# Kernel tuning notes

Measured on AMD Instinct MI355X. Metric: run time of the kernel, lower is better.

Reference implementation:

```python
import jax, jax.numpy as jnp
import numpy as np

B, S, E, H, FFN, NQ = 4, 2048, 1024, 16, 4096, 8
DK = E // H
EPS = 1e-5


def setup_inputs() -> dict:
    key = jax.random.key(0)
    ks = jax.random.split(key, 8)
    x = jax.random.normal(ks[0], (B, S, E), dtype=jnp.float32)
    theta = jax.random.normal(ks[1], (NQ,), dtype=jnp.float32)  # RY angles
    w1 = jax.random.normal(ks[2], (FFN, NQ), dtype=jnp.float32) / np.sqrt(NQ)
    b1 = jnp.zeros((FFN,), dtype=jnp.float32)
    w2 = jax.random.normal(ks[3], (E, FFN), dtype=jnp.float32) / np.sqrt(FFN)
    b2 = jnp.zeros((E,), dtype=jnp.float32)
    gamma1 = jnp.ones((E,), dtype=jnp.float32)
    beta1 = jnp.zeros((E,), dtype=jnp.float32)
    gamma2 = jnp.ones((E,), dtype=jnp.float32)
    beta2 = jnp.zeros((E,), dtype=jnp.float32)
    return {"x": x, "theta": theta, "w1": w1, "b1": b1, "w2": w2, "b2": b2,
            "gamma1": gamma1, "beta1": beta1, "gamma2": gamma2, "beta2": beta2}


def _layernorm(h, g, b):
    mu = jnp.mean(h, axis=-1, keepdims=True)
    var = jnp.mean(jnp.square(h - mu), axis=-1, keepdims=True)
    return (h - mu) * jax.lax.rsqrt(var + EPS) * g + b


def _attention(x):
    # q = k = v = separate_heads(x); no projection weights in the original.
    q = x.reshape(B, S, H, DK).transpose(0, 2, 1, 3)  # [B,H,S,DK]
    scores = jnp.einsum("bhqd,bhkd->bhqk", q, q) / np.sqrt(DK)
    probs = jax.nn.softmax(scores, axis=-1)
    out = jnp.einsum("bhqk,bhkd->bhqd", probs, q)
    return out.transpose(0, 2, 1, 3).reshape(B, S, E)


def _ffn_quantum(h, theta, w1, b1, w2, b2):
    # Per-token circuit: RX(x_i) then RY(theta_i) on independent qubits,
    # measure PauliZ -> <Z_i> = cos(x_i) * cos(theta_i). Batched over all tokens.
    qout = jnp.cos(h[..., :NQ]) * jnp.cos(theta)  # [B,S,NQ]
    hid = jax.nn.relu(jnp.einsum("bsq,fq->bsf", qout, w1) + b1)
    return jnp.einsum("bsf,ef->bse", hid, w2) + b2


def reference(x, theta, w1, b1, w2, b2, gamma1, beta1, gamma2, beta2):
    attn_out = _attention(x)
    h = _layernorm(x + attn_out, gamma1, beta1)
    ffn_out = _ffn_quantum(h, theta, w1, b1, w2, b2)
    return _layernorm(h + ffn_out, gamma2, beta2)
```

## Files before the change

### kernel.cpp

```cpp
#include <hip/hip_runtime.h>


#define Bq 4
#define Sq 2048
#define Eq 1024
#define Hq 16
#define DKq 64
#define FFNq 4096
#define NQq 8
#define LOG2E 1.44269504f

typedef unsigned int u32;
typedef unsigned short u16;
typedef _Float16 f16;
typedef f16 f16x8 __attribute__((ext_vector_type(8)));
typedef __fp16 fp16x2 __attribute__((ext_vector_type(2)));
typedef float f32x4 __attribute__((ext_vector_type(4)));

#if __has_builtin(__builtin_amdgcn_exp2f)
#define EXP2F __builtin_amdgcn_exp2f
#else
#define EXP2F exp2f
#endif

#define MFMA(a, b, c) __builtin_amdgcn_mfma_f32_16x16x32_f16((a), (b), (c), 0, 0, 0)

#define GLL(g, l)                                                          \
  __builtin_amdgcn_global_load_lds(                                        \
      (const __attribute__((address_space(1))) u32*)(g),                   \
      (__attribute__((address_space(3))) u32*)(l), 16, 0, 0)

__device__ __forceinline__ u16 f2h(float x) {
  f16 t = (f16)x;
  return __builtin_bit_cast(u16, t);
}
__device__ __forceinline__ float h2f(u16 w) {
  return (float)__builtin_bit_cast(f16, w);
}
#if __has_builtin(__builtin_amdgcn_cvt_pkrtz)
__device__ __forceinline__ u32 pkrtz(float a, float b) {
  fp16x2 r = __builtin_amdgcn_cvt_pkrtz(a, b);
  return __builtin_bit_cast(u32, r);
}
#else
__device__ __forceinline__ u32 pkrtz(float a, float b) {
  return (u32)f2h(a) | ((u32)f2h(b) << 16);
}
#endif

union F8 { f16x8 v; u32 w[4]; u16 h[8]; f16 e[8]; };

__global__ void k_cvt(const float* __restrict__ src, uint4* __restrict__ dst, int n8) {
  int i = blockIdx.x * 256 + threadIdx.x;
  if (i >= n8) return;
  const float4* s = (const float4*)src + 2 * (long)i;
  float4 a = s[0], b = s[1];
  uint4 r;
  r.x = pkrtz(a.x, a.y);
  r.y = pkrtz(a.z, a.w);
  r.z = pkrtz(b.x, b.y);
  r.w = pkrtz(b.z, b.w);
  dst[i] = r;
}

__global__ void k_prep(const float* __restrict__ x, u16* __restrict__ xh,
                       u16* __restrict__ xt) {
  __shared__ u16 tile[64 * 72];
  const int tid = threadIdx.x;
  const int bx = blockIdx.x;
  const int sb = bx & 31, bh = bx >> 5;
  const int b = bh >> 4, h = bh & 15;
  const int s0 = sb * 64;
  const int r = tid >> 2, cq = tid & 3;
  const float* xp = x + ((long)(b * Sq + s0 + r)) * Eq + h * 64 + cq * 16;
  float4 f0 = ((const float4*)xp)[0], f1 = ((const float4*)xp)[1];
  float4 f2 = ((const float4*)xp)[2], f3 = ((const float4*)xp)[3];
  u32 w[8];
  w[0] = pkrtz(f0.x, f0.y); w[1] = pkrtz(f0.z, f0.w);
  w[2] = pkrtz(f1.x, f1.y); w[3] = pkrtz(f1.z, f1.w);
  w[4] = pkrtz(f2.x, f2.y); w[5] = pkrtz(f2.z, f2.w);
  w[6] = pkrtz(f3.x, f3.y); w[7] = pkrtz(f3.z, f3.w);
  uint4* xo = (uint4*)(xh + ((long)(b * Sq + s0 + r)) * Eq + h * 64 + cq * 16);
  xo[0] = make_uint4(w[0], w[1], w[2], w[3]);
  xo[1] = make_uint4(w[4], w[5], w[6], w[7]);
  uint4* tp = (uint4*)(tile + r * 72 + cq * 16);
  tp[0] = make_uint4(w[0], w[1], w[2], w[3]);
  tp[1] = make_uint4(w[4], w[5], w[6], w[7]);
  __syncthreads();
  const int d = tid >> 2, rq = tid & 3;
  u32 o[8];
#pragma unroll
  for (int i = 0; i < 8; ++i) {
    u32 lo = tile[(rq * 16 + 2 * i) * 72 + d];
    u32 hi = tile[(rq * 16 + 2 * i + 1) * 72 + d];
    o[i] = lo | (hi << 16);
  }
  uint4* to = (uint4*)(xt + ((long)(bh * 64 + d)) * Sq + s0 + rq * 16);
  to[0] = make_uint4(o[0], o[1], o[2], o[3]);
  to[1] = make_uint4(o[4], o[5], o[6], o[7]);
}

__global__ __launch_bounds__(256) void k_attn(const u16* __restrict__ xh,
                                              const u16* __restrict__ xt,
                                              u16* __restrict__ attn) {
  __shared__ __align__(16) u16 lds[16384];
  u16* Kl = lds;
  u16* Vt = lds + 4096;
  u16* Pl = lds + 8192;

  const int tid = threadIdx.x;
  const int wave = tid >> 6, lane = tid & 63;
  const int n = lane & 15, quad = lane >> 4;

  const int bx = blockIdx.x;
  const int qb = bx >> 6, bh = bx & 63;
  const int b = bh >> 4, h = bh & 15;

  const u16* xh_bh = xh + (long)b * Sq * Eq + h * 64;
  const u16* xt_bh = xt + (long)bh * 64 * Sq;

  const float SC = 0.125f * LOG2E;
  F8 qf[2][2];
  float shift[2];
#pragma unroll
  for (int nt = 0; nt < 2; ++nt) {
    const int q = qb * 128 + wave * 32 + nt * 16 + n;
    const u16* qp = xh_bh + (long)q * Eq + quad * 8;
    F8 a, c;
    a.v = *(const f16x8*)qp;
    c.v = *(const f16x8*)(qp + 32);
    float s2 = 0.f;
#pragma unroll
    for (int i = 0; i < 8; ++i) {
      float va = (float)a.e[i], vc = (float)c.e[i];
      s2 += va * va + vc * vc;
      qf[nt][0].e[i] = a.e[i] * (f16)SC;
      qf[nt][1].e[i] = c.e[i] * (f16)SC;
    }
    s2 += __shfl_xor(s2, 16);
    s2 += __shfl_xor(s2, 32);
    shift[nt] = SC * s2;
  }

  const int r8 = lane >> 3;
  const int cl = (lane & 7) ^ r8;
  const u16* gK0 = xh_bh + (long)(wave * 16 + r8) * Eq + cl * 8;
  const u16* gK1 = gK0 + 8 * Eq;
  const u16* gV0 = xt_bh + (long)(wave * 16 + r8) * Sq + cl * 8;
  const u16* gV1 = gV0 + 8 * Sq;
  u16* lK0 = Kl + wave * 1024;
  u16* lK1 = lK0 + 512;
  u16* lV0 = Vt + wave * 1024;
  u16* lV1 = lV0 + 512;

  f32x4 O[2][4] = {};
  f32x4 lC[2] = {};
  const f16x8 vones = {(f16)1, (f16)1, (f16)1, (f16)1,
                       (f16)1, (f16)1, (f16)1, (f16)1};
  u16* Pw0 = Pl + (wave * 2 + 0) * 1024;
  u16* Pw1 = Pl + (wave * 2 + 1) * 1024;

  for (int kb = 0; kb < Sq / 64; ++kb) {
    __syncthreads();
    GLL(gK0, lK0); GLL(gK1, lK1);
    GLL(gV0, lV0); GLL(gV1, lV1);
    gK0 += 64 * Eq; gK1 += 64 * Eq; gV0 += 64; gV1 += 64;
    __syncthreads();

    f32x4 ST[2][4];
#pragma unroll
    for (int nt = 0; nt < 2; ++nt) {
      const float ms = -shift[nt];
#pragma unroll
      for (int mt = 0; mt < 4; ++mt) {
        ST[nt][mt][0] = ms; ST[nt][mt][1] = ms;
        ST[nt][mt][2] = ms; ST[nt][mt][3] = ms;
      }
    }
#pragma unroll
    for (int mt = 0; mt < 4; ++mt) {
#pragma unroll
      for (int c = 0; c < 2; ++c) {
        f16x8 af = *(const f16x8*)(Kl + (mt * 16 + n) * 64 +
                                   (((c * 4 + quad) ^ (n & 7)) * 8));
        ST[0][mt] = MFMA(af, qf[0][c].v, ST[0][mt]);
        ST[1][mt] = MFMA(af, qf[1][c].v, ST[1][mt]);
      }
    }

#pragma unroll
    for (int nt = 0; nt < 2; ++nt) {
      u16* Pw = nt ? Pw1 : Pw0;
#pragma unroll
      for (int mt = 0; mt < 4; ++mt) {
        float p0 = EXP2F(ST[nt][mt][0]);
        float p1 = EXP2F(ST[nt][mt][1]);
        float p2 = EXP2F(ST[nt][mt][2]);
        float p3 = EXP2F(ST[nt][mt][3]);
        const int ch = 2 * mt + (quad >> 1);
        *(uint2*)(Pw + n * 64 + ((ch ^ (n & 7)) * 8) + (quad & 1) * 4) =
            make_uint2(pkrtz(p0, p1), pkrtz(p2, p3));
      }
    }

#pragma unroll
    for (int c = 0; c < 2; ++c) {
      const int pc = ((c * 4 + quad) ^ (n & 7)) * 8;
      f16x8 pf0 = *(const f16x8*)(Pw0 + n * 64 + pc);
      f16x8 pf1 = *(const f16x8*)(Pw1 + n * 64 + pc);
      lC[0] = MFMA(vones, pf0, lC[0]);
      lC[1] = MFMA(vones, pf1, lC[1]);
#pragma unroll
      for (int dt = 0; dt < 4; ++dt) {
        f16x8 vf = *(const f16x8*)(Vt + (dt * 16 + n) * 64 + pc);
        O[0][dt] = MFMA(vf, pf0, O[0][dt]);
        O[1][dt] = MFMA(vf, pf1, O[1][dt]);
      }
    }
  }

#pragma unroll
  for (int nt = 0; nt < 2; ++nt) {
    const float inv = 1.0f / lC[nt][0];
    const int q = qb * 128 + wave * 32 + nt * 16 + n;
    u16* op = attn + (long)b * Sq * Eq + (long)q * Eq + h * 64;
#pragma unroll
    for (int dt = 0; dt < 4; ++dt) {
      u32 w0 = pkrtz(O[nt][dt][0] * inv, O[nt][dt][1] * inv);
      u32 w1 = pkrtz(O[nt][dt][2] * inv, O[nt][dt][3] * inv);
      *(uint2*)(op + dt * 16 + quad * 4) = make_uint2(w0, w1);
    }
  }
}

__global__ void k_ln1(const u16* __restrict__ xh, const u16* __restrict__ attn,
                      const float* __restrict__ g, const float* __restrict__ be,
                      const float* __restrict__ theta, u16* __restrict__ hout,
                      u16* __restrict__ qout) {
  const long t = blockIdx.x;
  const int tid = threadIdx.x;
  uint2 xw = ((const uint2*)(xh + t * Eq))[tid];
  uint2 aw = ((const uint2*)(attn + t * Eq))[tid];
  float v0 = h2f(xw.x & 0xffff) + h2f(aw.x & 0xffff);
  float v1 = h2f(xw.x >> 16) + h2f(aw.x >> 16);
  float v2 = h2f(xw.y & 0xffff) + h2f(aw.y & 0xffff);
  float v3 = h2f(xw.y >> 16) + h2f(aw.y >> 16);
  float s = (v0 + v1) + (v2 + v3);
  float s2 = v0 * v0 + v1 * v1 + v2 * v2 + v3 * v3;
#pragma unroll
  for (int o = 1; o < 64; o <<= 1) {
    s += __shfl_xor(s, o);
    s2 += __shfl_xor(s2, o);
  }
  __shared__ float red[8];
  const int wv = tid >> 6, ln = tid & 63;
  if (ln == 0) { red[wv] = s; red[4 + wv] = s2; }
  __syncthreads();
  s = red[0] + red[1] + red[2] + red[3];
  s2 = red[4] + red[5] + red[6] + red[7];
  const float mu = s * (1.f / Eq);
  const float var = s2 * (1.f / Eq) - mu * mu;
  const float rstd = rsqrtf(var + 1e-5f);
  float4 gv = ((const float4*)g)[tid];
  float4 bv = ((const float4*)be)[tid];
  float o0 = (v0 - mu) * rstd * gv.x + bv.x;
  float o1 = (v1 - mu) * rstd * gv.y + bv.y;
  float o2 = (v2 - mu) * rstd * gv.z + bv.z;
  float o3 = (v3 - mu) * rstd * gv.w + bv.w;
  ((uint2*)(hout + t * Eq))[tid] = make_uint2(pkrtz(o0, o1), pkrtz(o2, o3));
  if (tid < 2) {
    float hv[4] = {o0, o1, o2, o3};
    float q[4];
#pragma unroll
    for (int i = 0; i < 4; ++i) q[i] = cosf(hv[i]) * cosf(theta[tid * 4 + i]);
    *(uint2*)(qout + t * NQq + tid * 4) = make_uint2(pkrtz(q[0], q[1]), pkrtz(q[2], q[3]));
  }
}

__global__ void k_hid(const u16* __restrict__ qout, const float* __restrict__ w1,
                      const float* __restrict__ b1, u16* __restrict__ hid) {
  __shared__ float qs[256][8];
  const int tid = threadIdx.x;
  const int fb = blockIdx.x & 63, tb = blockIdx.x >> 6;
  const int f0 = fb * 64, t0 = tb * 256;
  {
    uint4 qw = *(const uint4*)(qout + (long)(t0 + tid) * NQq);
    qs[tid][0] = h2f(qw.x & 0xffff); qs[tid][1] = h2f(qw.x >> 16);
    qs[tid][2] = h2f(qw.y & 0xffff); qs[tid][3] = h2f(qw.y >> 16);
    qs[tid][4] = h2f(qw.z & 0xffff); qs[tid][5] = h2f(qw.z >> 16);
    qs[tid][6] = h2f(qw.w & 0xffff); qs[tid][7] = h2f(qw.w >> 16);
  }
  __syncthreads();
  const int wave = tid >> 6, lane = tid & 63;
  const int f = f0 + lane;
  const float4* wp = (const float4*)(w1 + (long)f * NQq);
  float4 wa = wp[0], wb = wp[1];
  const float bb = b1[f];
  const int trow = wave * 64;
  u16* op = hid + (long)(t0 + trow) * FFNq + f;
#pragma unroll 4
  for (int i = 0; i < 64; ++i) {
    const float* q = qs[trow + i];
    float acc = bb + q[0] * wa.x + q[1] * wa.y + q[2] * wa.z + q[3] * wa.w +
                q[4] * wb.x + q[5] * wb.y + q[6] * wb.z + q[7] * wb.w;
    acc = fmaxf(acc, 0.f);
    op[(long)i * FFNq] = f2h(acc);
  }
}

__global__ __launch_bounds__(256) void k_gemm(const u16* __restrict__ Ah,
                                              const u16* __restrict__ Bh,
                                              u16* __restrict__ C0,
                                              u16* __restrict__ C1) {
  __shared__ __align__(16) u16 lds[16384];
  u16* La = lds;
  u16* Lb = lds + 8192;
  const int tid = threadIdx.x;
  const int wave = tid >> 6, lane = tid & 63;
  const int n = lane & 15, quad = lane >> 4;
  const int wm = wave >> 1, wn = wave & 1;
  const int bxx = blockIdx.x;
  const int kk = bxx >> 9;
  const int bx = bxx & 511;
  const int m0 = (bx >> 3) * 128;
  const int n0 = (bx & 7) * 128;
  const int k0 = kk * (FFNq / 2);
  const int r8 = lane >> 3;
  const int cl = (lane & 7) ^ r8;

  const u16* gA[4];
  const u16* gB[4];
  u16* lA[4];
  u16* lB[4];
#pragma unroll
  for (int j = 0; j < 4; ++j) {
    const int row = wave * 32 + j * 8;
    gA[j] = Ah + (long)(m0 + row + r8) * FFNq + k0 + cl * 8;
    gB[j] = Bh + (long)(n0 + row + r8) * FFNq + k0 + cl * 8;
    lA[j] = La + row * 64;
    lB[j] = Lb + row * 64;
  }

  f32x4 acc[4][4] = {};
  for (int it = 0; it < FFNq / 2 / 64; ++it) {
    __syncthreads();
#pragma unroll
    for (int j = 0; j < 4; ++j) {
      GLL(gA[j], lA[j]);
      GLL(gB[j], lB[j]);
      gA[j] += 64;
      gB[j] += 64;
    }
    __syncthreads();
#pragma unroll
    for (int c = 0; c < 2; ++c) {
      f16x8 af[4], bf[4];
#pragma unroll
      for (int i = 0; i < 4; ++i) {
        const int ra = wm * 64 + i * 16 + n;
        const int rb = wn * 64 + i * 16 + n;
        af[i] = *(const f16x8*)(La + ra * 64 + (((c * 4 + quad) ^ (n & 7)) * 8));
        bf[i] = *(const f16x8*)(Lb + rb * 64 + (((c * 4 + quad) ^ (n & 7)) * 8));
      }
#pragma unroll
      for (int i = 0; i < 4; ++i)
#pragma unroll
        for (int j = 0; j < 4; ++j) acc[i][j] = MFMA(af[i], bf[j], acc[i][j]);
    }
  }
  u16* C = kk ? C1 : C0;
#pragma unroll
  for (int i = 0; i < 4; ++i) {
    const int row = m0 + wm * 64 + i * 16 + quad * 4;
#pragma unroll
    for (int j = 0; j < 4; ++j) {
      u16* cp = C + (long)row * Eq + n0 + wn * 64 + j * 16 + n;
      cp[0] = f2h(acc[i][j][0]);
      cp[Eq] = f2h(acc[i][j][1]);
      cp[2 * Eq] = f2h(acc[i][j][2]);
      cp[3 * Eq] = f2h(acc[i][j][3]);
    }
  }
}

__global__ void k_ln2(const u16* __restrict__ hin, const u16* __restrict__ p0f,
                      const u16* __restrict__ p1f, const float* __restrict__ b2,
                      const float* __restrict__ g, const float* __restrict__ be,
                      float* __restrict__ out) {
  const long t = blockIdx.x;
  const int tid = threadIdx.x;
  uint2 hw = ((const uint2*)(hin + t * Eq))[tid];
  uint2 fw = ((const uint2*)(p0f + t * Eq))[tid];
  uint2 ew = ((const uint2*)(p1f + t * Eq))[tid];
  float4 b2v = ((const float4*)b2)[tid];
  float v0 = h2f(hw.x & 0xffff) + h2f(fw.x & 0xffff) + h2f(ew.x & 0xffff) + b2v.x;
  float v1 = h2f(hw.x >> 16) + h2f(fw.x >> 16) + h2f(ew.x >> 16) + b2v.y;
  float v2 = h2f(hw.y & 0xffff) + h2f(fw.y & 0xffff) + h2f(ew.y & 0xffff) + b2v.z;
  float v3 = h2f(hw.y >> 16) + h2f(fw.y >> 16) + h2f(ew.y >> 16) + b2v.w;
  float s = (v0 + v1) + (v2 + v3);
  float s2 = v0 * v0 + v1 * v1 + v2 * v2 + v3 * v3;
#pragma unroll
  for (int o = 1; o < 64; o <<= 1) {
    s += __shfl_xor(s, o);
    s2 += __shfl_xor(s2, o);
  }
  __shared__ float red[8];
  const int wv = tid >> 6, ln = tid & 63;
  if (ln == 0) { red[wv] = s; red[4 + wv] = s2; }
  __syncthreads();
  s = red[0] + red[1] + red[2] + red[3];
  s2 = red[4] + red[5] + red[6] + red[7];
  const float mu = s * (1.f / Eq);
  const float var = s2 * (1.f / Eq) - mu * mu;
  const float rstd = rsqrtf(var + 1e-5f);
  float4 gv = ((const float4*)g)[tid];
  float4 bv = ((const float4*)be)[tid];
  float4 o;
  o.x = (v0 - mu) * rstd * gv.x + bv.x;
  o.y = (v1 - mu) * rstd * gv.y + bv.y;
  o.z = (v2 - mu) * rstd * gv.z + bv.z;
  o.w = (v3 - mu) * rstd * gv.w + bv.w;
  ((float4*)(out + t * Eq))[tid] = o;
}

extern "C" void kernel_launch(void* const* d_in, const int* in_sizes, int n_in,
                              void* d_out, int out_size, void* d_ws, size_t ws_size,
                              hipStream_t stream) {
  const float* x = (const float*)d_in[0];
  const float* theta = (const float*)d_in[1];
  const float* w1 = (const float*)d_in[2];
  const float* b1 = (const float*)d_in[3];
  const float* w2 = (const float*)d_in[4];
  const float* b2 = (const float*)d_in[5];
  const float* g1 = (const float*)d_in[6];
  const float* be1 = (const float*)d_in[7];
  const float* g2 = (const float*)d_in[8];
  const float* be2 = (const float*)d_in[9];
  float* out = (float*)d_out;

  char* ws = (char*)d_ws;
  u16* attn = (u16*)(ws);
  u16* h = (u16*)(ws + 16777216);
  u16* xh = (u16*)(ws + 33554432);
  u16* xt = (u16*)(ws + 50331648);
  u16* ffn0 = (u16*)(ws + 67108864);
  u16* ffn1 = (u16*)(ws + 83886080);
  u16* hid = (u16*)(ws + 100663296);
  u16* w2h = (u16*)(ws + 167772160);
  u16* qout = (u16*)(ws + 176160768);

  k_prep<<<Bq * Hq * (Sq / 64), 256, 0, stream>>>(x, xh, xt);
  k_cvt<<<2048, 256, 0, stream>>>(w2, (uint4*)w2h, (Eq * FFNq) / 8);
  k_attn<<<Bq * Hq * (Sq / 128), 256, 0, stream>>>(xh, xt, attn);
  k_ln1<<<Bq * Sq, 256, 0, stream>>>(xh, attn, g1, be1, theta, h, qout);
  k_hid<<<(Bq * Sq / 256) * (FFNq / 64), 256, 0, stream>>>(qout, w1, b1, hid);
  k_gemm<<<2 * (Bq * Sq / 128) * (Eq / 128), 256, 0, stream>>>(hid, w2h, ffn0, ffn1);
  k_ln2<<<Bq * Sq, 256, 0, stream>>>(h, ffn0, ffn1, b2, g2, be2, out);
}
```

Measured before the change: 348.0 us.

## Double-buffer K/V tiles in attention and widen k_hid to four features per thread

After: 344.8 us. No clear change (-0.9%).

```diff
diff --git a/kernel.cpp b/kernel.cpp
--- a/kernel.cpp
+++ b/kernel.cpp
@@ -103,10 +103,8 @@
 __global__ __launch_bounds__(256) void k_attn(const u16* __restrict__ xh,
                                               const u16* __restrict__ xt,
                                               u16* __restrict__ attn) {
-  __shared__ __align__(16) u16 lds[16384];
-  u16* Kl = lds;
-  u16* Vt = lds + 4096;
-  u16* Pl = lds + 8192;
+  __shared__ __align__(16) u16 lds[24576];
+  u16* Pl = lds + 16384;
 
   const int tid = threadIdx.x;
   const int wave = tid >> 6, lane = tid & 63;
@@ -148,24 +146,32 @@
   const u16* gK1 = gK0 + 8 * Eq;
   const u16* gV0 = xt_bh + (long)(wave * 16 + r8) * Sq + cl * 8;
   const u16* gV1 = gV0 + 8 * Sq;
-  u16* lK0 = Kl + wave * 1024;
-  u16* lK1 = lK0 + 512;
-  u16* lV0 = Vt + wave * 1024;
-  u16* lV1 = lV0 + 512;
+  const int lK0 = wave * 1024, lK1 = lK0 + 512;
+  const int lV0 = 4096 + wave * 1024, lV1 = lV0 + 512;
+
+  u16* cur = lds;
+  u16* nxt = lds + 8192;
+
+  GLL(gK0, cur + lK0); GLL(gK1, cur + lK1);
+  GLL(gV0, cur + lV0); GLL(gV1, cur + lV1);
+  gK0 += 64 * Eq; gK1 += 64 * Eq; gV0 += 64; gV1 += 64;
 
   f32x4 O[2][4] = {};
   f32x4 lC[2] = {};
   const f16x8 vones = {(f16)1, (f16)1, (f16)1, (f16)1,
                        (f16)1, (f16)1, (f16)1, (f16)1};
-  u16* Pw0 = Pl + (wave * 2 + 0) * 1024;
-  u16* Pw1 = Pl + (wave * 2 + 1) * 1024;
+  u16* Pw0 = Pl + wave * 2048;
+  u16* Pw1 = Pw0 + 1024;
 
   for (int kb = 0; kb < Sq / 64; ++kb) {
     __syncthreads();
-    GLL(gK0, lK0); GLL(gK1, lK1);
-    GLL(gV0, lV0); GLL(gV1, lV1);
-    gK0 += 64 * Eq; gK1 += 64 * Eq; gV0 += 64; gV1 += 64;
-    __syncthreads();
+    if (kb < Sq / 64 - 1) {
+      GLL(gK0, nxt + lK0); GLL(gK1, nxt + lK1);
+      GLL(gV0, nxt + lV0); GLL(gV1, nxt + lV1);
+      gK0 += 64 * Eq; gK1 += 64 * Eq; gV0 += 64; gV1 += 64;
+    }
+    u16* Kl = cur;
+    u16* Vt = cur + 4096;
 
     f32x4 ST[2][4];
 #pragma unroll
@@ -217,6 +223,7 @@
         O[1][dt] = MFMA(vf, pf1, O[1][dt]);
       }
     }
+    u16* t = cur; cur = nxt; nxt = t;
   }
 
 #pragma unroll
@@ -281,8 +288,8 @@
                       const float* __restrict__ b1, u16* __restrict__ hid) {
   __shared__ float qs[256][8];
   const int tid = threadIdx.x;
-  const int fb = blockIdx.x & 63, tb = blockIdx.x >> 6;
-  const int f0 = fb * 64, t0 = tb * 256;
+  const int fb = blockIdx.x & 15, tb = blockIdx.x >> 4;
+  const int f0 = fb * 256, t0 = tb * 256;
   {
     uint4 qw = *(const uint4*)(qout + (long)(t0 + tid) * NQq);
     qs[tid][0] = h2f(qw.x & 0xffff); qs[tid][1] = h2f(qw.x >> 16);
@@ -290,21 +297,32 @@
     qs[tid][4] = h2f(qw.z & 0xffff); qs[tid][5] = h2f(qw.z >> 16);
     qs[tid][6] = h2f(qw.w & 0xffff); qs[tid][7] = h2f(qw.w >> 16);
   }
+  const int wave = tid >> 6, lane = tid & 63;
+  const int f = f0 + lane * 4;
+  float4 wr[4][2];
+#pragma unroll
+  for (int r = 0; r < 4; ++r) {
+    const float4* wp = (const float4*)(w1 + (long)(f + r) * NQq);
+    wr[r][0] = wp[0];
+    wr[r][1] = wp[1];
+  }
+  float4 bb = *(const float4*)(b1 + f);
+  const float bbr[4] = {bb.x, bb.y, bb.z, bb.w};
   __syncthreads();
-  const int wave = tid >> 6, lane = tid & 63;
-  const int f = f0 + lane;
-  const float4* wp = (const float4*)(w1 + (long)f * NQq);
-  float4 wa = wp[0], wb = wp[1];
-  const float bb = b1[f];
   const int trow = wave * 64;
   u16* op = hid + (long)(t0 + trow) * FFNq + f;
-#pragma unroll 4
+#pragma unroll 2
   for (int i = 0; i < 64; ++i) {
     const float* q = qs[trow + i];
-    float acc = bb + q[0] * wa.x + q[1] * wa.y + q[2] * wa.z + q[3] * wa.w +
-                q[4] * wb.x + q[5] * wb.y + q[6] * wb.z + q[7] * wb.w;
-    acc = fmaxf(acc, 0.f);
-    op[(long)i * FFNq] = f2h(acc);
+    float acc[4];
+#pragma unroll
+    for (int r = 0; r < 4; ++r) {
+      acc[r] = bbr[r] + q[0] * wr[r][0].x + q[1] * wr[r][0].y + q[2] * wr[r][0].z +
+               q[3] * wr[r][0].w + q[4] * wr[r][1].x + q[5] * wr[r][1].y +
+               q[6] * wr[r][1].z + q[7] * wr[r][1].w;
+      acc[r] = fmaxf(acc[r], 0.f);
+    }
+    *(uint2*)(op + (long)i * FFNq) = make_uint2(pkrtz(acc[0], acc[1]), pkrtz(acc[2], acc[3]));
   }
 }
 
@@ -453,7 +471,7 @@
   k_cvt<<<2048, 256, 0, stream>>>(w2, (uint4*)w2h, (Eq * FFNq) / 8);
   k_attn<<<Bq * Hq * (Sq / 128), 256, 0, stream>>>(xh, xt, attn);
   k_ln1<<<Bq * Sq, 256, 0, stream>>>(xh, attn, g1, be1, theta, h, qout);
-  k_hid<<<(Bq * Sq / 256) * (FFNq / 64), 256, 0, stream>>>(qout, w1, b1, hid);
+  k_hid<<<(FFNq / 256) * (Bq * Sq / 256), 256, 0, stream>>>(qout, w1, b1, hid);
   k_gemm<<<2 * (Bq * Sq / 128) * (Eq / 128), 256, 0, stream>>>(hid, w2h, ffn0, ffn1);
   k_ln2<<<Bq * Sq, 256, 0, stream>>>(h, ffn0, ffn1, b2, g2, be2, out);
 }
```
